# Kernel tuning notes

Measured on AMD Instinct MI355X. Metric: run time of the kernel, lower is better.

Reference implementation:

```python
import jax, jax.numpy as jnp
import numpy as np

EPS = 1e-6

def setup_inputs() -> dict:
    key = jax.random.key(0)
    ks = jax.random.split(key, 7)
    T, B, S, A, D = 512, 32, 64, 8, 32
    x = jax.random.normal(ks[0], (T, B, D), dtype=jnp.float32)
    a = jax.random.normal(ks[1], (T, B, A), dtype=jnp.float32)
    mask = jnp.ones((T, B), dtype=jnp.float32)
    mu = jax.random.normal(ks[2], (S, D), dtype=jnp.float32)
    logv = 0.1 * jax.random.normal(ks[3], (S, D), dtype=jnp.float32)
    init_logits = jax.random.normal(ks[4], (S,), dtype=jnp.float32)
    w_base = 0.1 * jax.random.normal(ks[5], (S, S), dtype=jnp.float32)
    w_act = 0.1 * jax.random.normal(ks[6], (A, S, S), dtype=jnp.float32)
    return {"x": x, "a": a, "mask": mask, "mu": mu, "logv": logv,
            "init_logits": init_logits, "w_base": w_base, "w_act": w_act}

def reference(x, a, mask, mu, logv, init_logits, w_base, w_act):
    T, B, D = x.shape
    S = mu.shape[0]
    # Gaussian (diag) emission log-likelihood for every state: [T, B, S]
    var = jnp.exp(logv)
    diff = x[:, :, None, :] - mu  # [T, B, S, D]
    logp_x = -0.5 * jnp.sum(diff * diff / var + logv + jnp.log(2.0 * jnp.pi), axis=-1)
    # Logistic (action-conditioned) transition matrices for t=1..T-1: [T-1, B, S, S]
    trans = jax.nn.softmax(w_base + jnp.einsum('tba,aij->tbij', a[:-1], w_act), axis=-1)
    logp0 = jax.nn.log_softmax(init_logits)
    # alpha_0
    alpha0 = jax.nn.softmax(logp_x[0] + logp0, axis=-1)

    def fwd_step(b, inp):
        tr, lx = inp
        logp_z = jnp.log(jnp.sum(tr * b[:, :, None] + EPS, axis=-2))
        b_new = jax.nn.softmax(lx + logp_z, axis=-1)
        return b_new, b_new

    _, alpha_rest = jax.lax.scan(fwd_step, alpha0, (trans, logp_x[1:]))
    alpha = jnp.concatenate([alpha0[None], alpha_rest], axis=0)  # [T, B, S]

    log_trans = jnp.log(trans + EPS)

    def bwd_step(logb, inp):
        ltr, lx, m = inp
        new = jax.scipy.special.logsumexp(lx[:, None, :] + ltr + logb[:, None, :], axis=-1)
        new = new * (m[:, None] == 1)
        return new, new

    _, lb = jax.lax.scan(bwd_step, jnp.zeros((B, S), x.dtype),
                         (log_trans, logp_x[1:], mask[1:]), reverse=True)
    log_beta = jnp.concatenate([lb, jnp.zeros((1, B, S), x.dtype)], axis=0)  # [T, B, S]

    # Posterior state marginals
    q_z = jax.nn.softmax(jnp.log(alpha + EPS) + log_beta, axis=-1)
    return q_z
```

## Files before the change

kernel.cpp:

```cpp
#include <hip/hip_runtime.h>
#include <hip/hip_fp16.h>
#include <math.h>

#define TT 512
#define BB 32
#define SS 64
#define AA 8
#define DD 32
#define EPSF 1e-6f
#define SEPS (64.0f * 1e-6f)
#define TS 68

typedef _Float16 h2_t __attribute__((ext_vector_type(2)));
typedef __fp16   fp16v2 __attribute__((ext_vector_type(2)));

__device__ __forceinline__ int   f2i(float x){ return __float_as_int(x); }
__device__ __forceinline__ float i2f(int x){ return __int_as_float(x); }
__device__ __forceinline__ float readlane_f(float v, int l){
  return i2f(__builtin_amdgcn_readlane(f2i(v), l));
}
__device__ __forceinline__ h2_t i2h2(int x){ return __builtin_bit_cast(h2_t, x); }
__device__ __forceinline__ h2_t u2h2(unsigned x){ return __builtin_bit_cast(h2_t, x); }
__device__ __forceinline__ int pkrtz_i(float a, float b){
  fp16v2 p = __builtin_amdgcn_cvt_pkrtz(a, b);
  return __builtin_bit_cast(int, p);
}
template<int CTRL, int RMASK>
__device__ __forceinline__ float dpp_add(float x){
  return x + i2f(__builtin_amdgcn_update_dpp(0, f2i(x), CTRL, RMASK, 0xf, true));
}
__device__ __forceinline__ float wave_sum_dpp(float x){
  x = dpp_add<0x111, 0xf>(x);
  x = dpp_add<0x112, 0xf>(x);
  x = dpp_add<0x114, 0xf>(x);
  x = dpp_add<0x118, 0xf>(x);
  x = dpp_add<0x142, 0xa>(x);
  x = dpp_add<0x143, 0xc>(x);
  return readlane_f(x, 63);
}
__device__ __forceinline__ float dpp_xor1(float x){
  return i2f(__builtin_amdgcn_update_dpp(0, f2i(x), 0xB1, 0xf, 0xf, true));
}
__device__ __forceinline__ float wave_sum(float v){
  #pragma unroll
  for (int m = 1; m < 64; m <<= 1) v += __shfl_xor(v, m, 64);
  return v;
}
__device__ __forceinline__ float wave_max(float v){
  #pragma unroll
  for (int m = 1; m < 64; m <<= 1) v = fmaxf(v, __shfl_xor(v, m, 64));
  return v;
}
#define BARRIER() asm volatile("s_waitcnt lgkmcnt(0)\n\ts_barrier" ::: "memory")
#define LGKM0()   asm volatile("s_waitcnt lgkmcnt(0)" ::: "memory")

__device__ __forceinline__ unsigned pk2(float a, float b){
  return (unsigned)__half_as_ushort(__float2half_rn(a))
       | ((unsigned)__half_as_ushort(__float2half_rn(b)) << 16);
}

#if __has_builtin(__builtin_amdgcn_fdot2)
#define FDOT2(A, B, C) __builtin_amdgcn_fdot2((A), (B), (C), false)
#else
__device__ __forceinline__ float fdot2_emul(h2_t a, h2_t b, float c){
  return fmaf((float)a.x, (float)b.x, fmaf((float)a.y, (float)b.y, c));
}
#define FDOT2(A, B, C) fdot2_emul((A), (B), (C))
#endif

__global__ void prep_kernel(const float* __restrict__ logv,
                            float* __restrict__ iv, float* __restrict__ cs){
  int gid = blockIdx.x * blockDim.x + threadIdx.x;
  if (gid < SS * DD) iv[gid] = __expf(-logv[gid]);
  if (gid < SS){
    float s = 0.f;
    #pragma unroll
    for (int d = 0; d < DD; ++d) s += logv[gid * DD + d];
    cs[gid] = s + (float)DD * 1.8378770664093453f;
  }
}

__global__ __launch_bounds__(256) void logpx_kernel(
    const float* __restrict__ x, const float* __restrict__ mu,
    const float* __restrict__ iv, const float* __restrict__ cs,
    float* __restrict__ slx_out){
  const int lane = threadIdx.x & 63;
  const int w = threadIdx.x >> 6;
  const int row = blockIdx.x * 4 + w;
  const float* __restrict__ xp  = x  + row * DD;
  const float* __restrict__ mup = mu + lane * DD;
  const float* __restrict__ ivp = iv + lane * DD;
  float acc = 0.f;
  #pragma unroll
  for (int d = 0; d < DD; ++d){
    float diff = xp[d] - mup[d];
    acc = fmaf(diff * diff, ivp[d], acc);
  }
  float lx = -0.5f * (acc + cs[lane]);
  float mx = wave_max(lx);
  slx_out[row * SS + lane] = lx - mx;
}

__global__ __launch_bounds__(512) void trans_kernel(
    const float* __restrict__ a, const float* __restrict__ w_base,
    const float* __restrict__ w_act, unsigned short* __restrict__ trans, int F){
  const int b  = blockIdx.x >> 4;
  const int tc = blockIdx.x & 15;
  const int t0 = tc * 32;
  const int q    = threadIdx.x >> 6;
  const int j    = threadIdx.x & 63;
  __shared__ float aS[32 * 8];
  __shared__ float red[8][8][68];
  if (threadIdx.x < 256)
    aS[threadIdx.x] = a[(((t0 + (threadIdx.x >> 3)) * BB) + b) * AA + (threadIdx.x & 7)];
  float wb[8], wa[8][8];
  #pragma unroll
  for (int e = 0; e < 8; ++e){
    wb[e] = w_base[(8 * q + e) * SS + j];
    #pragma unroll
    for (int k = 0; k < 8; ++k)
      wa[k][e] = w_act[(k * SS + 8 * q + e) * SS + j];
  }
  __syncthreads();
  const int er = j & 7;
  const int g8 = (j >> 3) * 8;
  int rem = F - t0;
  const int nt = (rem < 0) ? 0 : (rem < 32 ? rem : 32);
  for (int tt = 0; tt < nt; ++tt){
    float aa[8];
    #pragma unroll
    for (int k = 0; k < 8; ++k) aa[k] = aS[tt * 8 + k];
    float ev[8];
    #pragma unroll
    for (int e = 0; e < 8; ++e){
      float u = wb[e];
      #pragma unroll
      for (int k = 0; k < 8; ++k) u = fmaf(aa[k], wa[k][e], u);
      ev[e] = __expf(u);
    }
    #pragma unroll
    for (int e = 0; e < 8; ++e) red[q][e][j] = ev[e];
    LGKM0();
    float4 p0 = *(const float4*)&red[q][er][g8];
    float4 p1 = *(const float4*)&red[q][er][g8 + 4];
    float part = ((p0.x + p0.y) + (p0.z + p0.w)) + ((p1.x + p1.y) + (p1.z + p1.w));
    part += __shfl_xor(part, 8, 64);
    part += __shfl_xor(part, 16, 64);
    part += __shfl_xor(part, 32, 64);
    float ri = __builtin_amdgcn_rcpf(part);
    float re[8];
    #pragma unroll
    for (int e = 0; e < 8; ++e) re[e] = readlane_f(ri, e);
    uint4 o;
    o.x = pk2(ev[0] * re[0], ev[1] * re[1]);
    o.y = pk2(ev[2] * re[2], ev[3] * re[3]);
    o.z = pk2(ev[4] * re[4], ev[5] * re[5]);
    o.w = pk2(ev[6] * re[6], ev[7] * re[7]);
    *(uint4*)(trans + ((size_t)(t0 + tt) * BB + b) * (SS * SS) + q * 512 + j * 8) = o;
  }
}

__global__ __launch_bounds__(64, 1) void scan_wave_kernel(
    const float* __restrict__ slx, const float* __restrict__ mask,
    const float* __restrict__ il, const unsigned short* __restrict__ trans,
    float* __restrict__ alpha, float* __restrict__ log_beta){
  const int lane = threadIdx.x;
  const bool is_fwd = (blockIdx.x < BB);
  const int b = is_fwd ? blockIdx.x : (blockIdx.x - BB);

  __shared__ __align__(16) int Ltr[2][32 * 68];

#define LOADT(ARR, t) do{ \
    const uint4* p_ = (const uint4*)(trans + ((size_t)(t) * BB + b) * (SS * SS) + lane * 8); \
    _Pragma("unroll") \
    for (int q_ = 0; q_ < 8; ++q_) ARR[q_] = p_[q_ * 64]; \
  }while(0)

  if (is_fwd){
    uint4 A[8], B[8], C[8], D[8], E[8], F[8], G[8];
#define DOTQ(ARR, Q) \
    a0 = FDOT2(i2h2(__builtin_amdgcn_readlane(upki, 8*Q + 0)), u2h2(ARR[Q].x), a0); \
    a1 = FDOT2(i2h2(__builtin_amdgcn_readlane(upki, 8*Q + 2)), u2h2(ARR[Q].y), a1); \
    a2 = FDOT2(i2h2(__builtin_amdgcn_readlane(upki, 8*Q + 4)), u2h2(ARR[Q].z), a2); \
    a3 = FDOT2(i2h2(__builtin_amdgcn_readlane(upki, 8*Q + 6)), u2h2(ARR[Q].w), a3);
#define DOTS(ARR) \
    DOTQ(ARR,0) DOTQ(ARR,1) DOTQ(ARR,2) DOTQ(ARR,3) \
    DOTQ(ARR,4) DOTQ(ARR,5) DOTQ(ARR,6) DOTQ(ARR,7)

    LOADT(A, 0); LOADT(B, 1); LOADT(C, 2); LOADT(D, 3);
    LOADT(E, 4); LOADT(F, 5); LOADT(G, 6);
    float u = __expf(slx[b * SS + lane] + il[lane]);
    float c = __builtin_amdgcn_rcpf(wave_sum_dpp(u));
    alpha[b * SS + lane] = u * c;
    float slxn = slx[(BB + b) * SS + lane];

#define FBODY(s_, ARR, DOL, DOS) { \
    float elxc = __expf(slxn); \
    if (DOS) slxn = slx[(((s_) + 2) * BB + b) * SS + lane]; \
    float usw = dpp_xor1(u); \
    int upki = pkrtz_i(u, usw); \
    float a0 = 0.f, a1 = 0.f, a2 = 0.f, a3 = 0.f; \
    DOTS(ARR); \
    if (DOL) LOADT(ARR, (s_) + 7); \
    float S_ = (a0 + a1) + (a2 + a3); \
    u = elxc * fmaf(c, S_, SEPS); \
    c = __builtin_amdgcn_rcpf(wave_sum_dpp(u)); \
    alpha[(((s_) + 1) * BB + b) * SS + lane] = u * c; }

    for (int s = 0; s < 504; s += 7){
      FBODY(s + 0, A, 1, 1)
      FBODY(s + 1, B, 1, 1)
      FBODY(s + 2, C, 1, 1)
      FBODY(s + 3, D, 1, 1)
      FBODY(s + 4, E, 1, 1)
      FBODY(s + 5, F, 1, 1)
      FBODY(s + 6, G, 1, 1)
    }
    FBODY(504, A, 0, 1)
    FBODY(505, B, 0, 1)
    FBODY(506, C, 0, 1)
    FBODY(507, D, 0, 1)
    FBODY(508, E, 0, 1)
    FBODY(509, F, 0, 1)
    FBODY(510, G, 0, 0)
  } else {
    uint4 R0[8], R1[8];
#define WLDS(SL, R) do{ \
    int* Lp_ = &Ltr[SL][lane]; \
    _Pragma("unroll") \
    for (int q_ = 0; q_ < 8; ++q_){ \
      Lp_[(4*q_ + 0) * 68] = (int)R[q_].x; \
      Lp_[(4*q_ + 1) * 68] = (int)R[q_].y; \
      Lp_[(4*q_ + 2) * 68] = (int)R[q_].z; \
      Lp_[(4*q_ + 3) * 68] = (int)R[q_].w; \
    } \
  }while(0)

    LOADT(R0, TT - 2);
    WLDS(0, R0);
    LOADT(R0, TT - 3);
    LOADT(R1, TT - 4);
    float pcar = 1.0f;
    log_beta[((TT - 1) * BB + b) * SS + lane] = 0.f;
    float elxc = __expf(slx[((TT - 1) * BB + b) * SS + lane]);
    float sxn1 = slx[((TT - 2) * BB + b) * SS + lane];
    float sxn2 = slx[((TT - 3) * BB + b) * SS + lane];
    float mkc  = mask[(TT - 1) * BB + b];
    float mkn1 = mask[(TT - 2) * BB + b];
    float mkn2 = mask[(TT - 3) * BB + b];
    const int sel = (lane & 1) ? 0x07060302 : 0x05040100;

#define BBODY(s_, RB, DOW, DOL, DOP) { \
    const int t_ = TT - 2 - (s_); \
    int4 w4[16]; \
    { const int4* rp_ = (const int4*)&Ltr[(s_) & 1][(lane >> 1) * 68]; \
      _Pragma("unroll") \
      for (int k_ = 0; k_ < 16; ++k_) w4[k_] = rp_[k_]; } \
    float wgt = elxc * pcar; \
    float wsw = dpp_xor1(wgt); \
    int wpki = pkrtz_i(wgt, wsw); \
    float W_ = wave_sum_dpp(wgt); \
    float rW_ = __builtin_amdgcn_rcpf(W_); \
    if (DOW) WLDS(((s_) + 1) & 1, RB); \
    if (DOL) LOADT(RB, t_ - 3); \
    float mcur = mkc; \
    float elxn = __expf(sxn1); \
    sxn1 = sxn2; mkc = mkn1; mkn1 = mkn2; \
    if (DOP){ \
      sxn2 = slx[((t_ - 2) * BB + b) * SS + lane]; \
      mkn2 = mask[(t_ - 2) * BB + b]; \
    } \
    int hh[32]; const int* wd_ = (const int*)w4; \
    _Pragma("unroll") \
    for (int m_ = 0; m_ < 32; ++m_) \
      hh[m_] = (int)__builtin_amdgcn_perm((unsigned)wd_[2*m_ + 1], (unsigned)wd_[2*m_], (unsigned)sel); \
    float a0 = 0.f, a1 = 0.f, a2 = 0.f, a3 = 0.f; \
    _Pragma("unroll") \
    for (int m_ = 0; m_ < 32; m_ += 4){ \
      a0 = FDOT2(i2h2(__builtin_amdgcn_readlane(wpki, 2*m_ + 0)), i2h2(hh[m_ + 0]), a0); \
      a1 = FDOT2(i2h2(__builtin_amdgcn_readlane(wpki, 2*m_ + 2)), i2h2(hh[m_ + 1]), a1); \
      a2 = FDOT2(i2h2(__builtin_amdgcn_readlane(wpki, 2*m_ + 4)), i2h2(hh[m_ + 2]), a2); \
      a3 = FDOT2(i2h2(__builtin_amdgcn_readlane(wpki, 2*m_ + 6)), i2h2(hh[m_ + 3]), a3); \
    } \
    float S_ = (a0 + a1) + (a2 + a3); \
    float pv_ = fmaf(S_, rW_, EPSF); \
    pcar = (mcur == 1.0f) ? pv_ : 1.0f; \
    log_beta[(t_ * BB + b) * SS + lane] = __logf(pcar); \
    elxc = elxn; }

    for (int s = 0; s < 508; s += 2){
      BBODY(s + 0, R0, 1, 1, 1)
      BBODY(s + 1, R1, 1, 1, 1)
    }
    BBODY(508, R0, 1, 0, 1)
    BBODY(509, R1, 1, 0, 0)
    BBODY(510, R0, 0, 0, 0)
  }
}

__global__ __launch_bounds__(768) void scan_kernel(
    const float* __restrict__ slx, const float* __restrict__ mask,
    const float* __restrict__ il, const float* __restrict__ a,
    const float* __restrict__ w_base, const float* __restrict__ w_act,
    float* __restrict__ alpha, float* __restrict__ log_beta){
  const int lane = threadIdx.x & 63;
  const int w    = threadIdx.x >> 6;
  const bool is_fwd = (blockIdx.x < BB);
  const int b = is_fwd ? blockIdx.x : (blockIdx.x - BB);

  __shared__ __align__(16) float tile[3][SS * TS];
  __shared__ float rsp[3][8][SS];
  __shared__ float fpart[2][4][SS];
  __shared__ __align__(16) float aLDS[TT * AA];
  __shared__ float mLDS[TT];

  for (int idx = threadIdx.x; idx < TT * AA; idx += 768){
    int t = idx >> 3, k = idx & 7;
    aLDS[idx] = a[(t * BB + b) * AA + k];
  }
  for (int idx = threadIdx.x; idx < TT; idx += 768)
    mLDS[idx] = mask[idx * BB + b];

  if (w >= 4){
    const int pw = w - 4;
    const int jb = pw * 8;
    float wb[8], wa[8][8];
    #pragma unroll
    for (int jj = 0; jj < 8; ++jj){
      wb[jj] = w_base[lane * SS + jb + jj];
      #pragma unroll
      for (int k = 0; k < 8; ++k)
        wa[k][jj] = w_act[(k * SS + lane) * SS + jb + jj];
    }
    float aa[8], aan[8];
    {
      const int t0 = is_fwd ? 0 : (TT - 2);
      const float* __restrict__ ap = a + (t0 * BB + b) * AA;
      #pragma unroll
      for (int k = 0; k < 8; ++k) aa[k] = ap[k];
      const int t1 = is_fwd ? 1 : (TT - 3);
      const float* __restrict__ ap1 = a + (t1 * BB + b) * AA;
      #pragma unroll
      for (int k = 0; k < 8; ++k) aan[k] = ap1[k];
    }
    {
      float ev[8]; float racc = 0.f;
      #pragma unroll
      for (int jj = 0; jj < 8; ++jj){
        float u = wb[jj];
        #pragma unroll
        for (int k = 0; k < 8; ++k) u = fmaf(aa[k], wa[k][jj], u);
        ev[jj] = __expf(u); racc += ev[jj];
      }
      *(float4*)&tile[0][lane * TS + jb]     = make_float4(ev[0],ev[1],ev[2],ev[3]);
      *(float4*)&tile[0][lane * TS + jb + 4] = make_float4(ev[4],ev[5],ev[6],ev[7]);
      rsp[0][pw][lane] = racc;
    }
    BARRIER();
    int tw = 1;
    for (int s = 0; s < TT - 1; ++s){
      if (s <= TT - 3){
        #pragma unroll
        for (int k = 0; k < 8; ++k) aa[k] = aan[k];
        if (s + 1 <= TT - 3){
          const int tn = is_fwd ? (s + 2) : (TT - 4 - s);
          #pragma unroll
          for (int k = 0; k < 8; ++k) aan[k] = aLDS[tn * AA + k];
        }
        float ev[8]; float racc = 0.f;
        #pragma unroll
        for (int jj = 0; jj < 8; ++jj){
          float u = wb[jj];
          #pragma unroll
          for (int k = 0; k < 8; ++k) u = fmaf(aa[k], wa[k][jj], u);
          ev[jj] = __expf(u); racc += ev[jj];
        }
        *(float4*)&tile[tw][lane * TS + jb]     = make_float4(ev[0],ev[1],ev[2],ev[3]);
        *(float4*)&tile[tw][lane * TS + jb + 4] = make_float4(ev[4],ev[5],ev[6],ev[7]);
        rsp[tw][pw][lane] = racc;
        tw = (tw == 2) ? 0 : tw + 1;
      }
      BARRIER();
    }
  } else if (is_fwd){
    const int wb16 = __builtin_amdgcn_readfirstlane(w * 16);
    float u = __expf(slx[b * SS + lane] + il[lane]);
    float c = __builtin_amdgcn_rcpf(wave_sum_dpp(u));
    if (w == 0) alpha[b * SS + lane] = u * c;
    float slxn = slx[(BB + b) * SS + lane];
    float elxc = 0.f;
    BARRIER();
    int ts = 0;
    for (int s = 0; s < TT - 1; ++s){
      if (s > 0){
        const int fs = (s - 1) & 1;
        float S = (fpart[fs][0][lane] + fpart[fs][1][lane])
                + (fpart[fs][2][lane] + fpart[fs][3][lane]);
        u = elxc * fmaf(c, S, SEPS);
        c = __builtin_amdgcn_rcpf(wave_sum_dpp(u));
        if (w == 0) alpha[(s * BB + b) * SS + lane] = u * c;
      }
      float rs = ((rsp[ts][0][lane] + rsp[ts][1][lane]) + (rsp[ts][2][lane] + rsp[ts][3][lane]))
               + ((rsp[ts][4][lane] + rsp[ts][5][lane]) + (rsp[ts][6][lane] + rsp[ts][7][lane]));
      float va = u * __builtin_amdgcn_rcpf(rs);
      const float* __restrict__ tp = &tile[ts][0];
      float a0 = 0.f, a1 = 0.f, a2 = 0.f, a3 = 0.f;
      #pragma unroll
      for (int r = 0; r < 16; r += 4){
        a0 = fmaf(readlane_f(va, wb16 + r    ), tp[(wb16 + r    ) * TS + lane], a0);
        a1 = fmaf(readlane_f(va, wb16 + r + 1), tp[(wb16 + r + 1) * TS + lane], a1);
        a2 = fmaf(readlane_f(va, wb16 + r + 2), tp[(wb16 + r + 2) * TS + lane], a2);
        a3 = fmaf(readlane_f(va, wb16 + r + 3), tp[(wb16 + r + 3) * TS + lane], a3);
      }
      fpart[s & 1][w][lane] = (a0 + a1) + (a2 + a3);
      elxc = __expf(slxn);
      if (s + 2 <= TT - 1) slxn = slx[((s + 2) * BB + b) * SS + lane];
      ts = (ts == 2) ? 0 : ts + 1;
      BARRIER();
    }
    {
      const int fs = (TT - 2) & 1;
      float S = (fpart[fs][0][lane] + fpart[fs][1][lane])
              + (fpart[fs][2][lane] + fpart[fs][3][lane]);
      u = elxc * fmaf(c, S, SEPS);
      c = __builtin_amdgcn_rcpf(wave_sum_dpp(u));
      if (w == 0) alpha[((TT - 1) * BB + b) * SS + lane] = u * c;
    }
  } else {
    const int wb16 = __builtin_amdgcn_readfirstlane(w * 16);
    float breg = 0.f, rWc = 1.f;
    if (w == 0) log_beta[((TT - 1) * BB + b) * SS + lane] = 0.f;
    float slxc = slx[((TT - 1) * BB + b) * SS + lane];
    float mprev = 1.f;
    BARRIER();
    int ts = 0, pts = 2;
    for (int s = 0; s < TT - 1; ++s){
      if (s > 0){
        const int fs = (s - 1) & 1;
        float eh = (fpart[fs][0][lane] + fpart[fs][1][lane])
                 + (fpart[fs][2][lane] + fpart[fs][3][lane]);
        float rsv = ((rsp[pts][0][lane] + rsp[pts][1][lane]) + (rsp[pts][2][lane] + rsp[pts][3][lane]))
                  + ((rsp[pts][4][lane] + rsp[pts][5][lane]) + (rsp[pts][6][lane] + rsp[pts][7][lane]));
        float v = __logf(fmaf(eh * __builtin_amdgcn_rcpf(rsv), rWc, EPSF));
        breg = (mprev == 1.0f) ? v : 0.0f;
        if (w == 0) log_beta[((TT - 1 - s) * BB + b) * SS + lane] = breg;
      }
      float wgt = __expf(slxc + breg);
      float W = wave_sum_dpp(wgt);
      rWc = __builtin_amdgcn_rcpf(W);
      const float* __restrict__ tp = &tile[ts][lane * TS + wb16];
      float4 e0 = *(const float4*)(tp);
      float4 e1 = *(const float4*)(tp + 4);
      float4 e2 = *(const float4*)(tp + 8);
      float4 e3 = *(const float4*)(tp + 12);
      float a0 = 0.f, a1 = 0.f, a2 = 0.f, a3 = 0.f;
      a0 = fmaf(readlane_f(wgt, wb16 + 0),  e0.x, a0);
      a1 = fmaf(readlane_f(wgt, wb16 + 1),  e0.y, a1);
      a2 = fmaf(readlane_f(wgt, wb16 + 2),  e0.z, a2);
      a3 = fmaf(readlane_f(wgt, wb16 + 3),  e0.w, a3);
      a0 = fmaf(readlane_f(wgt, wb16 + 4),  e1.x, a0);
      a1 = fmaf(readlane_f(wgt, wb16 + 5),  e1.y, a1);
      a2 = fmaf(readlane_f(wgt, wb16 + 6),  e1.z, a2);
      a3 = fmaf(readlane_f(wgt, wb16 + 7),  e1.w, a3);
      a0 = fmaf(readlane_f(wgt, wb16 + 8),  e2.x, a0);
      a1 = fmaf(readlane_f(wgt, wb16 + 9),  e2.y, a1);
      a2 = fmaf(readlane_f(wgt, wb16 + 10), e2.z, a2);
      a3 = fmaf(readlane_f(wgt, wb16 + 11), e2.w, a3);
      a0 = fmaf(readlane_f(wgt, wb16 + 12), e3.x, a0);
      a1 = fmaf(readlane_f(wgt, wb16 + 13), e3.y, a1);
      a2 = fmaf(readlane_f(wgt, wb16 + 14), e3.z, a2);
      a3 = fmaf(readlane_f(wgt, wb16 + 15), e3.w, a3);
      fpart[s & 1][w][lane] = (a0 + a1) + (a2 + a3);
      mprev = mLDS[TT - 1 - s];
      if (s <= TT - 3) slxc = slx[((TT - 2 - s) * BB + b) * SS + lane];
      pts = ts; ts = (ts == 2) ? 0 : ts + 1;
      BARRIER();
    }
    {
      const int fs = (TT - 2) & 1;
      float eh = (fpart[fs][0][lane] + fpart[fs][1][lane])
               + (fpart[fs][2][lane] + fpart[fs][3][lane]);
      float rsv = ((rsp[pts][0][lane] + rsp[pts][1][lane]) + (rsp[pts][2][lane] + rsp[pts][3][lane]))
                + ((rsp[pts][4][lane] + rsp[pts][5][lane]) + (rsp[pts][6][lane] + rsp[pts][7][lane]));
      float v = __logf(fmaf(eh * __builtin_amdgcn_rcpf(rsv), rWc, EPSF));
      breg = (mprev == 1.0f) ? v : 0.0f;
      if (w == 0) log_beta[b * SS + lane] = breg;
    }
  }
}

__global__ __launch_bounds__(256) void qz_kernel(
    const float* __restrict__ alpha, const float* __restrict__ log_beta,
    float* __restrict__ out){
  const int lane = threadIdx.x & 63;
  const int w = threadIdx.x >> 6;
  const int row = blockIdx.x * 4 + w;
  float v = __logf(alpha[row * SS + lane] + EPSF) + log_beta[row * SS + lane];
  float mx = wave_max(v);
  float e = __expf(v - mx);
  float sm = wave_sum(e);
  out[row * SS + lane] = e * __builtin_amdgcn_rcpf(sm);
}

extern "C" void kernel_launch(void* const* d_in, const int* in_sizes, int n_in,
                              void* d_out, int out_size, void* d_ws, size_t ws_size,
                              hipStream_t stream){
  const float* x      = (const float*)d_in[0];
  const float* a      = (const float*)d_in[1];
  const float* mask   = (const float*)d_in[2];
  const float* mu     = (const float*)d_in[3];
  const float* logv   = (const float*)d_in[4];
  const float* il     = (const float*)d_in[5];
  const float* w_base = (const float*)d_in[6];
  const float* w_act  = (const float*)d_in[7];
  float* out = (float*)d_out;

  float* ws = (float*)d_ws;
  const size_t TBS = (size_t)TT * BB * SS;
  float* iv       = ws;
  float* cs       = ws + 2048;
  float* slx      = ws + 4096;
  float* alpha    = slx + TBS;
  float* log_beta = alpha + TBS;
  unsigned short* trans = (unsigned short*)(log_beta + TBS);

  const size_t base_bytes = ((size_t)4096 + 3 * TBS) * 4;
  const size_t full_bytes = base_bytes + (size_t)(TT - 1) * BB * SS * SS * 2;

  prep_kernel<<<8, 256, 0, stream>>>(logv, iv, cs);
  logpx_kernel<<<TT * BB / 4, 256, 0, stream>>>(x, mu, iv, cs, slx);
  if (ws_size >= full_bytes){
    trans_kernel<<<512, 512, 0, stream>>>(a, w_base, w_act, trans, TT - 1);
    scan_wave_kernel<<<2 * BB, 64, 0, stream>>>(slx, mask, il, trans,
                                                alpha, log_beta);
  } else {
    scan_kernel<<<2 * BB, 768, 0, stream>>>(slx, mask, il, a, w_base, w_act,
                                            alpha, log_beta);
  }
  qz_kernel<<<TT * BB / 4, 256, 0, stream>>>(alpha, log_beta, out);
}
```

Measured before the change: 381.8 us.

## Replace LDS transpose in backward scan with register multiply and cross-lane shuffle reduction

The backward wave scan no longer stages each transition tile through LDS for a transpose. Each lane now multiplies its register-resident fp16 rows by its own weight and reduces across lanes with xor-shuffle trees, first in packed half and then in float. The loads use an XOR-swizzled chunk order so each lane ends up holding the right output slot, and prefetch depth goes from two to four tiles. This removes the LDS write/read round trip and its barrier-free serialization per step, at the cost of many shuffles and some extra fp16 accumulation error.

```diff
diff --git a/kernel.cpp b/kernel.cpp
--- a/kernel.cpp
+++ b/kernel.cpp
@@ -21,6 +21,8 @@
 }
 __device__ __forceinline__ h2_t i2h2(int x){ return __builtin_bit_cast(h2_t, x); }
 __device__ __forceinline__ h2_t u2h2(unsigned x){ return __builtin_bit_cast(h2_t, x); }
+__device__ __forceinline__ __half2 h2bits(int x){ return __builtin_bit_cast(__half2, x); }
+__device__ __forceinline__ int bitsh2(__half2 x){ return __builtin_bit_cast(int, x); }
 __device__ __forceinline__ int pkrtz_i(float a, float b){
   fp16v2 p = __builtin_amdgcn_cvt_pkrtz(a, b);
   return __builtin_bit_cast(int, p);
@@ -168,8 +170,6 @@
   const bool is_fwd = (blockIdx.x < BB);
   const int b = is_fwd ? blockIdx.x : (blockIdx.x - BB);
 
-  __shared__ __align__(16) int Ltr[2][32 * 68];
-
 #define LOADT(ARR, t) do{ \
     const uint4* p_ = (const uint4*)(trans + ((size_t)(t) * BB + b) * (SS * SS) + lane * 8); \
     _Pragma("unroll") \
@@ -224,22 +224,21 @@
     FBODY(509, F, 0, 1)
     FBODY(510, G, 0, 0)
   } else {
-    uint4 R0[8], R1[8];
-#define WLDS(SL, R) do{ \
-    int* Lp_ = &Ltr[SL][lane]; \
-    _Pragma("unroll") \
-    for (int q_ = 0; q_ < 8; ++q_){ \
-      Lp_[(4*q_ + 0) * 68] = (int)R[q_].x; \
-      Lp_[(4*q_ + 1) * 68] = (int)R[q_].y; \
-      Lp_[(4*q_ + 2) * 68] = (int)R[q_].z; \
-      Lp_[(4*q_ + 3) * 68] = (int)R[q_].w; \
-    } \
+    const int qx = (lane >> 3) & 7;
+    const bool j0 = (lane & 1) != 0;
+    const bool j1 = (lane & 2) != 0;
+    const bool j2 = (lane & 4) != 0;
+    uint4 RA[8], RB_[8], RC[8], RD[8];
+#define LOADTX(ARR, t) do{ \
+    const unsigned short* bp_ = trans + ((size_t)(t) * BB + b) * (SS * SS) + lane * 8; \
+    _Pragma("unroll") \
+    for (int q_ = 0; q_ < 8; ++q_) ARR[q_] = *(const uint4*)(bp_ + (size_t)(q_ ^ qx) * 512); \
   }while(0)
 
-    LOADT(R0, TT - 2);
-    WLDS(0, R0);
-    LOADT(R0, TT - 3);
-    LOADT(R1, TT - 4);
+    LOADTX(RA, TT - 2);
+    LOADTX(RB_, TT - 3);
+    LOADTX(RC, TT - 4);
+    LOADTX(RD, TT - 5);
     float pcar = 1.0f;
     log_beta[((TT - 1) * BB + b) * SS + lane] = 0.f;
     float elxc = __expf(slx[((TT - 1) * BB + b) * SS + lane]);
@@ -248,21 +247,50 @@
     float mkc  = mask[(TT - 1) * BB + b];
     float mkn1 = mask[(TT - 2) * BB + b];
     float mkn2 = mask[(TT - 3) * BB + b];
-    const int sel = (lane & 1) ? 0x07060302 : 0x05040100;
-
-#define BBODY(s_, RB, DOW, DOL, DOP) { \
+
+#define BBODY(s_, RR, DOL, DOP) { \
     const int t_ = TT - 2 - (s_); \
-    int4 w4[16]; \
-    { const int4* rp_ = (const int4*)&Ltr[(s_) & 1][(lane >> 1) * 68]; \
-      _Pragma("unroll") \
-      for (int k_ = 0; k_ < 16; ++k_) w4[k_] = rp_[k_]; } \
     float wgt = elxc * pcar; \
-    float wsw = dpp_xor1(wgt); \
-    int wpki = pkrtz_i(wgt, wsw); \
     float W_ = wave_sum_dpp(wgt); \
     float rW_ = __builtin_amdgcn_rcpf(W_); \
-    if (DOW) WLDS(((s_) + 1) & 1, RB); \
-    if (DOL) LOADT(RB, t_ - 3); \
+    __half2 wh = h2bits(pkrtz_i(wgt, wgt)); \
+    __half2 sv[32]; \
+    _Pragma("unroll") \
+    for (int q_ = 0; q_ < 8; ++q_){ \
+      sv[4*q_+0] = __hmul2(h2bits((int)RR[q_].x), wh); \
+      sv[4*q_+1] = __hmul2(h2bits((int)RR[q_].y), wh); \
+      sv[4*q_+2] = __hmul2(h2bits((int)RR[q_].z), wh); \
+      sv[4*q_+3] = __hmul2(h2bits((int)RR[q_].w), wh); \
+    } \
+    if (DOL) LOADTX(RR, t_ - 4); \
+    _Pragma("unroll") \
+    for (int k_ = 0; k_ < 16; ++k_) \
+      sv[k_] = __hadd2(sv[k_], h2bits(__shfl_xor(bitsh2(sv[k_+16]), 32, 64))); \
+    _Pragma("unroll") \
+    for (int k_ = 0; k_ < 8; ++k_) \
+      sv[k_] = __hadd2(sv[k_], h2bits(__shfl_xor(bitsh2(sv[k_+8]), 16, 64))); \
+    _Pragma("unroll") \
+    for (int k_ = 0; k_ < 4; ++k_) \
+      sv[k_] = __hadd2(sv[k_], h2bits(__shfl_xor(bitsh2(sv[k_+4]), 8, 64))); \
+    float f_[8]; \
+    _Pragma("unroll") \
+    for (int k_ = 0; k_ < 4; ++k_){ \
+      f_[2*k_]     = __low2float(sv[k_]); \
+      f_[2*k_ + 1] = __high2float(sv[k_]); \
+    } \
+    _Pragma("unroll") \
+    for (int k_ = 0; k_ < 8; ++k_) f_[k_] += __shfl_xor(f_[k_], 4, 64); \
+    _Pragma("unroll") \
+    for (int k_ = 0; k_ < 8; ++k_) f_[k_] += __shfl_xor(f_[k_], 2, 64); \
+    _Pragma("unroll") \
+    for (int k_ = 0; k_ < 8; ++k_) f_[k_] += __shfl_xor(f_[k_], 1, 64); \
+    float e0_ = j0 ? f_[1] : f_[0]; \
+    float e1_ = j0 ? f_[3] : f_[2]; \
+    float e2_ = j0 ? f_[5] : f_[4]; \
+    float e3_ = j0 ? f_[7] : f_[6]; \
+    float g0_ = j1 ? e1_ : e0_; \
+    float g1_ = j1 ? e3_ : e2_; \
+    float S_  = j2 ? g1_ : g0_; \
     float mcur = mkc; \
     float elxn = __expf(sxn1); \
     sxn1 = sxn2; mkc = mkn1; mkn1 = mkn2; \
@@ -270,31 +298,24 @@
       sxn2 = slx[((t_ - 2) * BB + b) * SS + lane]; \
       mkn2 = mask[(t_ - 2) * BB + b]; \
     } \
-    int hh[32]; const int* wd_ = (const int*)w4; \
-    _Pragma("unroll") \
-    for (int m_ = 0; m_ < 32; ++m_) \
-      hh[m_] = (int)__builtin_amdgcn_perm((unsigned)wd_[2*m_ + 1], (unsigned)wd_[2*m_], (unsigned)sel); \
-    float a0 = 0.f, a1 = 0.f, a2 = 0.f, a3 = 0.f; \
-    _Pragma("unroll") \
-    for (int m_ = 0; m_ < 32; m_ += 4){ \
-      a0 = FDOT2(i2h2(__builtin_amdgcn_readlane(wpki, 2*m_ + 0)), i2h2(hh[m_ + 0]), a0); \
-      a1 = FDOT2(i2h2(__builtin_amdgcn_readlane(wpki, 2*m_ + 2)), i2h2(hh[m_ + 1]), a1); \
-      a2 = FDOT2(i2h2(__builtin_amdgcn_readlane(wpki, 2*m_ + 4)), i2h2(hh[m_ + 2]), a2); \
-      a3 = FDOT2(i2h2(__builtin_amdgcn_readlane(wpki, 2*m_ + 6)), i2h2(hh[m_ + 3]), a3); \
-    } \
-    float S_ = (a0 + a1) + (a2 + a3); \
     float pv_ = fmaf(S_, rW_, EPSF); \
     pcar = (mcur == 1.0f) ? pv_ : 1.0f; \
     log_beta[(t_ * BB + b) * SS + lane] = __logf(pcar); \
     elxc = elxn; }
 
-    for (int s = 0; s < 508; s += 2){
-      BBODY(s + 0, R0, 1, 1, 1)
-      BBODY(s + 1, R1, 1, 1, 1)
-    }
-    BBODY(508, R0, 1, 0, 1)
-    BBODY(509, R1, 1, 0, 0)
-    BBODY(510, R0, 0, 0, 0)
+    for (int s = 0; s < 504; s += 4){
+      BBODY(s + 0, RA,  1, 1)
+      BBODY(s + 1, RB_, 1, 1)
+      BBODY(s + 2, RC,  1, 1)
+      BBODY(s + 3, RD,  1, 1)
+    }
+    BBODY(504, RA,  1, 1)
+    BBODY(505, RB_, 1, 1)
+    BBODY(506, RC,  1, 1)
+    BBODY(507, RD,  0, 1)
+    BBODY(508, RA,  0, 1)
+    BBODY(509, RB_, 0, 0)
+    BBODY(510, RC,  0, 0)
   }
 }
 
```

New measurement: 872.6 us. 129% more time.
